# Performance work log

Hardware: AMD Instinct MI355X
Metric: run time of the kernel (lower is better)

The kernel has to match this reference:

```python
import jax, jax.numpy as jnp
import numpy as np

TS = 4  # tile_size


def _disp_upsample_slanted(d, dx, dy, ts):
    """Slanted-plane disparity upsample (PixelShuffle of per-tile-pixel planes).
    d, dx, dy: [B,1,Ht,Wt] -> full-res disparity [B,1,H,W], H=Ht*ts, W=Wt*ts.
    output[y,x] = d[y//ts,x//ts] + (y%ts - c)*dy + (x%ts - c)*dx, c=(ts-1)/2."""
    B, _, Ht, Wt = d.shape
    c = (ts - 1) / 2
    off = jnp.arange(ts, dtype=d.dtype) - jnp.asarray(c, d.dtype)  # [ts]
    d_, dx_, dy_ = d[:, 0], dx[:, 0], dy[:, 0]  # [B,Ht,Wt]
    off_i = off[None, :, None, None, None]  # row offset within tile
    off_j = off[None, None, :, None, None]  # col offset within tile
    disp = d_[:, None, None] + off_i * dy_[:, None, None] + off_j * dx_[:, None, None]
    # [B,ts_i,ts_j,Ht,Wt] -> pixel-shuffle -> [B,1,H,W]
    disp = disp.transpose(0, 3, 1, 4, 2).reshape(B, 1, Ht * ts, Wt * ts)
    return disp


def _l1_cost_chaos(fea_l, fea_r, disp):
    """Per-pixel horizontal warp of fea_r by continuous disparity (linear interp,
    zero outside image), then L1 distance over channels. Returns [B,1,H,W]."""
    B, C, H, W = fea_l.shape
    x = jnp.arange(W, dtype=disp.dtype)
    x_src = x[None, None, None, :] - disp              # [B,1,H,W]
    x0 = jnp.floor(x_src)
    w = (x_src - x0).astype(fea_r.dtype)
    x0i = jnp.clip(x0.astype(jnp.int32), 0, W - 1)
    x1i = jnp.clip(x0i + 1, 0, W - 1)
    f0 = jnp.take_along_axis(fea_r, jnp.broadcast_to(x0i, (B, C, H, W)), axis=3)
    f1 = jnp.take_along_axis(fea_r, jnp.broadcast_to(x1i, (B, C, H, W)), axis=3)
    warped = f0 * (1.0 - w) + f1 * w
    valid = (x_src >= 0) & (x_src <= W - 1)
    warped = jnp.where(valid, warped, jnp.zeros((), fea_r.dtype))
    return jnp.sum(jnp.abs(fea_l - warped), axis=1, keepdims=True)


def _tile_unshuffle(cv, ts):
    """[B,1,H,W] -> [B, ts*ts, H//ts, W//ts]; channel i*ts+j holds cv[i::ts, j::ts]."""
    B, _, H, W = cv.shape
    Ht, Wt = H // ts, W // ts
    return cv.reshape(B, Ht, ts, Wt, ts).transpose(0, 2, 4, 1, 3).reshape(B, ts * ts, Ht, Wt)


def setup_inputs() -> dict:
    key = jax.random.key(0)
    k1, k2, k3, k4, k5 = jax.random.split(key, 5)
    B, C, H, W, ts = 4, 32, 512, 960, TS
    Ht, Wt = H // ts, W // ts
    d = jax.random.uniform(k1, (B, 1, Ht, Wt), jnp.float32) * 48.0
    dx = jax.random.normal(k2, (B, 1, Ht, Wt), jnp.float32) * 0.1
    dy = jax.random.normal(k3, (B, 1, Ht, Wt), jnp.float32) * 0.1
    tile_plane = jnp.concatenate([d, dx, dy], axis=1)  # [B,3,Ht,Wt]
    fea_l = jax.random.normal(k4, (B, C, H, W), jnp.float32)
    fea_r = jax.random.normal(k5, (B, C, H, W), jnp.float32)
    return {"tile_plane": tile_plane, "fea_l": fea_l, "fea_r": fea_r}


def reference(tile_plane, fea_l, fea_r):
    ts = TS
    tile_d = tile_plane[:, 0:1]
    tile_dx = tile_plane[:, 1:2]
    tile_dy = tile_plane[:, 2:3]
    local_cv = []
    for disp_d in (-1, 0, 1):
        disp_full = _disp_upsample_slanted(tile_d + disp_d, tile_dx, tile_dy, ts)
        cv = _l1_cost_chaos(fea_l, fea_r, disp_full)        # [B,1,H,W]
        local_cv.append(_tile_unshuffle(cv, ts))            # [B,ts*ts,Ht,Wt]
    return jnp.concatenate(local_cv, axis=1)                # [B,3*ts*ts,Ht,Wt]
```

## Files before the change

kernel.cpp:

```cpp
#include <hip/hip_runtime.h>
#include <cstdint>

#define AS1 __attribute__((address_space(1)))
#define AS3 __attribute__((address_space(3)))

constexpr int B  = 4;
constexpr int C  = 32;
constexpr int H  = 512;
constexpr int Wd = 960;
constexpr int Ht = H / 4;
constexpr int Wt = Wd / 4;
constexpr int HW = H * Wd;

constexpr int BLKX  = 256;
constexpr int XMARG = 56;
constexpr int SELEM = BLKX + 64;

__global__ __launch_bounds__(256, 4) void tile_warping_kernel(
    const float* __restrict__ tp,
    const float* __restrict__ fl,
    const float* __restrict__ fr,
    float* __restrict__ out)
{
    __shared__ float sm[SELEM * C];

    const int lane = threadIdx.x;
    const int x0 = blockIdx.x * BLKX;
    const int y  = blockIdx.y;
    const int b  = blockIdx.z;
    const int xstart = x0 - XMARG;

    const float* frrow = fr + ((size_t)b * C * H + y) * Wd;
    #pragma unroll
    for (int chunk = 0; chunk < (SELEM * C) / (BLKX * 4); ++chunk) {
        int e   = chunk * (BLKX * 4) + lane * 4;
        int ch  = e / SELEM;
        int off = e - ch * SELEM;
        int gx  = min(max(xstart + off, 0), Wd - 4);
        const float* gp = frrow + (size_t)ch * HW + gx;
        __builtin_amdgcn_global_load_lds((const AS1 float*)gp,
                                         (AS3 float*)(&sm[e]), 16, 0, 0);
    }
    __syncthreads();

    const int x = x0 + lane;
    if (x < Wd) {
        const int ht = y >> 2, ii = y & 3;
        const int wt = x >> 2, jj = x & 3;

        const int tbase = ((b * 3) * Ht + ht) * Wt + wt;
        const float dv  = tp[tbase];
        const float dxv = tp[tbase + Ht * Wt];
        const float dyv = tp[tbase + 2 * Ht * Wt];

        const float oi = (float)ii - 1.5f;
        const float oj = (float)jj - 1.5f;

        int   o0[3];
        float w[3], w1[3];
        bool  val[3];
        #pragma unroll
        for (int k = 0; k < 3; ++k) {
            float disp = ((dv + (float)(k - 1)) + oi * dyv) + oj * dxv;
            float xs = (float)x - disp;
            float ff = floorf(xs);
            w[k]  = xs - ff;
            w1[k] = 1.0f - w[k];
            int c0 = min(max((int)ff, 0), Wd - 1);
            o0[k]  = c0 - xstart;
            val[k] = (xs >= 0.0f) && (xs <= (float)(Wd - 1));
        }

        const float* flp = fl + ((size_t)b * C * H + y) * Wd + x;

        float s0 = 0.f, s1 = 0.f, s2 = 0.f;
        #pragma unroll 4
        for (int c = 0; c < C; ++c) {
            float l = flp[(size_t)c * HW];
            const float* bp = sm + c * SELEM;
            float f00 = bp[o0[0]], f01 = bp[o0[0] + 1];
            float f10 = bp[o0[1]], f11 = bp[o0[1] + 1];
            float f20 = bp[o0[2]], f21 = bp[o0[2] + 1];
            float wv0 = val[0] ? (f00 * w1[0] + f01 * w[0]) : 0.f;
            float wv1 = val[1] ? (f10 * w1[1] + f11 * w[1]) : 0.f;
            float wv2 = val[2] ? (f20 * w1[2] + f21 * w[2]) : 0.f;
            s0 += fabsf(l - wv0);
            s1 += fabsf(l - wv1);
            s2 += fabsf(l - wv2);
        }

        const int obase = ((b * 48) * Ht + ht) * Wt + wt;
        out[obase + (0 * 16 + ii * 4 + jj) * (Ht * Wt)] = s0;
        out[obase + (1 * 16 + ii * 4 + jj) * (Ht * Wt)] = s1;
        out[obase + (2 * 16 + ii * 4 + jj) * (Ht * Wt)] = s2;
    }
}

extern "C" void kernel_launch(void* const* d_in, const int* in_sizes, int n_in,
                              void* d_out, int out_size, void* d_ws, size_t ws_size,
                              hipStream_t stream) {
    const float* tp = (const float*)d_in[0];
    const float* fl = (const float*)d_in[1];
    const float* fr = (const float*)d_in[2];
    float* out = (float*)d_out;

    dim3 grid((Wd + BLKX - 1) / BLKX, H, B);
    tile_warping_kernel<<<grid, 256, 0, stream>>>(tp, fl, fr, out);
}
```

Before: 493.7 us.

## Stage right-feature rows through LDS in two channel phases to raise occupancy

```diff
diff --git a/kernel.cpp b/kernel.cpp
--- a/kernel.cpp
+++ b/kernel.cpp
@@ -15,14 +15,17 @@
 constexpr int BLKX  = 256;
 constexpr int XMARG = 56;
 constexpr int SELEM = BLKX + 64;
+constexpr int CPH   = 16;
+constexpr int NPH   = C / CPH;
+constexpr int NCHUNK = (SELEM * CPH) / (BLKX * 4);
 
-__global__ __launch_bounds__(256, 4) void tile_warping_kernel(
+__global__ __launch_bounds__(256, 7) void tile_warping_kernel(
     const float* __restrict__ tp,
     const float* __restrict__ fl,
     const float* __restrict__ fr,
     float* __restrict__ out)
 {
-    __shared__ float sm[SELEM * C];
+    __shared__ float sm[SELEM * CPH];
 
     const int lane = threadIdx.x;
     const int x0 = blockIdx.x * BLKX;
@@ -31,8 +34,9 @@
     const int xstart = x0 - XMARG;
 
     const float* frrow = fr + ((size_t)b * C * H + y) * Wd;
+
     #pragma unroll
-    for (int chunk = 0; chunk < (SELEM * C) / (BLKX * 4); ++chunk) {
+    for (int chunk = 0; chunk < NCHUNK; ++chunk) {
         int e   = chunk * (BLKX * 4) + lane * 4;
         int ch  = e / SELEM;
         int off = e - ch * SELEM;
@@ -41,13 +45,20 @@
         __builtin_amdgcn_global_load_lds((const AS1 float*)gp,
                                          (AS3 float*)(&sm[e]), 16, 0, 0);
     }
-    __syncthreads();
 
-    const int x = x0 + lane;
-    if (x < Wd) {
-        const int ht = y >> 2, ii = y & 3;
-        const int wt = x >> 2, jj = x & 3;
+    const int x   = x0 + lane;
+    const bool act = (x < Wd);
 
+    const int ht = y >> 2, ii = y & 3;
+    const int wt = x >> 2, jj = x & 3;
+
+    int   o0[3];
+    float w[3], w1[3];
+    bool  val[3];
+    float s0 = 0.f, s1 = 0.f, s2 = 0.f;
+    const float* flp = fl + ((size_t)b * C * H + y) * Wd + x;
+
+    if (act) {
         const int tbase = ((b * 3) * Ht + ht) * Wt + wt;
         const float dv  = tp[tbase];
         const float dxv = tp[tbase + Ht * Wt];
@@ -56,9 +67,6 @@
         const float oi = (float)ii - 1.5f;
         const float oj = (float)jj - 1.5f;
 
-        int   o0[3];
-        float w[3], w1[3];
-        bool  val[3];
         #pragma unroll
         for (int k = 0; k < 3; ++k) {
             float disp = ((dv + (float)(k - 1)) + oi * dyv) + oj * dxv;
@@ -70,25 +78,56 @@
             o0[k]  = c0 - xstart;
             val[k] = (xs >= 0.0f) && (xs <= (float)(Wd - 1));
         }
+    } else {
+        o0[0] = o0[1] = o0[2] = 0;
+        w[0] = w[1] = w[2] = 0.f;
+        w1[0] = w1[1] = w1[2] = 0.f;
+        val[0] = val[1] = val[2] = false;
+    }
 
-        const float* flp = fl + ((size_t)b * C * H + y) * Wd + x;
-
-        float s0 = 0.f, s1 = 0.f, s2 = 0.f;
-        #pragma unroll 4
-        for (int c = 0; c < C; ++c) {
-            float l = flp[(size_t)c * HW];
-            const float* bp = sm + c * SELEM;
-            float f00 = bp[o0[0]], f01 = bp[o0[0] + 1];
-            float f10 = bp[o0[1]], f11 = bp[o0[1] + 1];
-            float f20 = bp[o0[2]], f21 = bp[o0[2] + 1];
-            float wv0 = val[0] ? (f00 * w1[0] + f01 * w[0]) : 0.f;
-            float wv1 = val[1] ? (f10 * w1[1] + f11 * w[1]) : 0.f;
-            float wv2 = val[2] ? (f20 * w1[2] + f21 * w[2]) : 0.f;
-            s0 += fabsf(l - wv0);
-            s1 += fabsf(l - wv1);
-            s2 += fabsf(l - wv2);
+    #pragma unroll
+    for (int p = 0; p < NPH; ++p) {
+        if (p) {
+            __syncthreads();
+            #pragma unroll
+            for (int chunk = 0; chunk < NCHUNK; ++chunk) {
+                int e   = chunk * (BLKX * 4) + lane * 4;
+                int ch  = e / SELEM;
+                int off = e - ch * SELEM;
+                int gx  = min(max(xstart + off, 0), Wd - 4);
+                const float* gp = frrow + (size_t)(p * CPH + ch) * HW + gx;
+                __builtin_amdgcn_global_load_lds((const AS1 float*)gp,
+                                                 (AS3 float*)(&sm[e]), 16, 0, 0);
+            }
         }
 
+        float l[CPH];
+        if (act) {
+            #pragma unroll
+            for (int c = 0; c < CPH; ++c)
+                l[c] = flp[(size_t)(p * CPH + c) * HW];
+        }
+
+        __syncthreads();
+
+        if (act) {
+            #pragma unroll
+            for (int c = 0; c < CPH; ++c) {
+                const float* bp = sm + c * SELEM;
+                float f00 = bp[o0[0]], f01 = bp[o0[0] + 1];
+                float f10 = bp[o0[1]], f11 = bp[o0[1] + 1];
+                float f20 = bp[o0[2]], f21 = bp[o0[2] + 1];
+                float wv0 = val[0] ? (f00 * w1[0] + f01 * w[0]) : 0.f;
+                float wv1 = val[1] ? (f10 * w1[1] + f11 * w[1]) : 0.f;
+                float wv2 = val[2] ? (f20 * w1[2] + f21 * w[2]) : 0.f;
+                s0 += fabsf(l[c] - wv0);
+                s1 += fabsf(l[c] - wv1);
+                s2 += fabsf(l[c] - wv2);
+            }
+        }
+    }
+
+    if (act) {
         const int obase = ((b * 48) * Ht + ht) * Wt + wt;
         out[obase + (0 * 16 + ii * 4 + jj) * (Ht * Wt)] = s0;
         out[obase + (1 * 16 + ii * 4 + jj) * (Ht * Wt)] = s1;
```

After: 850.4 us. 72.3% more time.

## Share one 4-tap LDS window across the three disparities and prefetch fea_l

Applied to the files above, without the earlier changes.

```diff
diff --git a/kernel.cpp b/kernel.cpp
--- a/kernel.cpp
+++ b/kernel.cpp
@@ -15,6 +15,7 @@
 constexpr int BLKX  = 256;
 constexpr int XMARG = 56;
 constexpr int SELEM = BLKX + 64;
+constexpr int NCHUNK = (SELEM * C) / (BLKX * 4);
 
 __global__ __launch_bounds__(256, 4) void tile_warping_kernel(
     const float* __restrict__ tp,
@@ -32,7 +33,7 @@
 
     const float* frrow = fr + ((size_t)b * C * H + y) * Wd;
     #pragma unroll
-    for (int chunk = 0; chunk < (SELEM * C) / (BLKX * 4); ++chunk) {
+    for (int chunk = 0; chunk < NCHUNK; ++chunk) {
         int e   = chunk * (BLKX * 4) + lane * 4;
         int ch  = e / SELEM;
         int off = e - ch * SELEM;
@@ -41,54 +42,74 @@
         __builtin_amdgcn_global_load_lds((const AS1 float*)gp,
                                          (AS3 float*)(&sm[e]), 16, 0, 0);
     }
+
+    const int x   = x0 + lane;
+    const bool act = (x < Wd);
+    const int xc  = act ? x : (Wd - 1);
+
+    const int ht = y >> 2, ii = y & 3;
+    const int wt = xc >> 2, jj = xc & 3;
+
+    const int tbase = ((b * 3) * Ht + ht) * Wt + wt;
+    const float dv  = tp[tbase];
+    const float dxv = tp[tbase + Ht * Wt];
+    const float dyv = tp[tbase + 2 * Ht * Wt];
+
+    const float oi = (float)ii - 1.5f;
+    const float oj = (float)jj - 1.5f;
+
+    const float disp_c = ((dv + 0.0f) + oi * dyv) + oj * dxv;
+    const float xs_c = (float)xc - disp_c;
+    const float xs0 = xs_c + 1.0f;
+    const float xs2 = xs_c - 1.0f;
+
+    const float ff = floorf(xs_c);
+    const float w  = xs_c - ff;
+    const float w1 = 1.0f - w;
+
+    const bool val0 = (xs0  >= 0.0f) && (xs0  <= (float)(Wd - 1));
+    const bool val1 = (xs_c >= 0.0f) && (xs_c <= (float)(Wd - 1));
+    const bool val2 = (xs2  >= 0.0f) && (xs2  <= (float)(Wd - 1));
+
+    const int iw = (int)ff - 1;
+    const int ow = min(max(iw - xstart, 0), SELEM - 4);
+
+    const float* flp = fl + ((size_t)b * C * H + y) * Wd + xc;
+
+    float la[8], lb[8];
+    #pragma unroll
+    for (int j = 0; j < 8; ++j)
+        la[j] = flp[(size_t)j * HW];
+
     __syncthreads();
 
-    const int x = x0 + lane;
-    if (x < Wd) {
-        const int ht = y >> 2, ii = y & 3;
-        const int wt = x >> 2, jj = x & 3;
+    float s0 = 0.f, s1 = 0.f, s2 = 0.f;
 
-        const int tbase = ((b * 3) * Ht + ht) * Wt + wt;
-        const float dv  = tp[tbase];
-        const float dxv = tp[tbase + Ht * Wt];
-        const float dyv = tp[tbase + 2 * Ht * Wt];
-
-        const float oi = (float)ii - 1.5f;
-        const float oj = (float)jj - 1.5f;
-
-        int   o0[3];
-        float w[3], w1[3];
-        bool  val[3];
+    #pragma unroll
+    for (int oct = 0; oct < 4; ++oct) {
+        float* cur = (oct & 1) ? lb : la;
+        float* nxt = (oct & 1) ? la : lb;
+        if (oct < 3) {
+            #pragma unroll
+            for (int j = 0; j < 8; ++j)
+                nxt[j] = flp[(size_t)((oct + 1) * 8 + j) * HW];
+        }
         #pragma unroll
-        for (int k = 0; k < 3; ++k) {
-            float disp = ((dv + (float)(k - 1)) + oi * dyv) + oj * dxv;
-            float xs = (float)x - disp;
-            float ff = floorf(xs);
-            w[k]  = xs - ff;
-            w1[k] = 1.0f - w[k];
-            int c0 = min(max((int)ff, 0), Wd - 1);
-            o0[k]  = c0 - xstart;
-            val[k] = (xs >= 0.0f) && (xs <= (float)(Wd - 1));
-        }
-
-        const float* flp = fl + ((size_t)b * C * H + y) * Wd + x;
-
-        float s0 = 0.f, s1 = 0.f, s2 = 0.f;
-        #pragma unroll 4
-        for (int c = 0; c < C; ++c) {
-            float l = flp[(size_t)c * HW];
-            const float* bp = sm + c * SELEM;
-            float f00 = bp[o0[0]], f01 = bp[o0[0] + 1];
-            float f10 = bp[o0[1]], f11 = bp[o0[1] + 1];
-            float f20 = bp[o0[2]], f21 = bp[o0[2] + 1];
-            float wv0 = val[0] ? (f00 * w1[0] + f01 * w[0]) : 0.f;
-            float wv1 = val[1] ? (f10 * w1[1] + f11 * w[1]) : 0.f;
-            float wv2 = val[2] ? (f20 * w1[2] + f21 * w[2]) : 0.f;
+        for (int j = 0; j < 8; ++j) {
+            const int c = oct * 8 + j;
+            const float* bp = sm + c * SELEM + ow;
+            float t0 = bp[0], t1 = bp[1], t2 = bp[2], t3 = bp[3];
+            float wv0 = val0 ? (t2 * w1 + t3 * w) : 0.f;
+            float wv1 = val1 ? (t1 * w1 + t2 * w) : 0.f;
+            float wv2 = val2 ? (t0 * w1 + t1 * w) : 0.f;
+            float l = cur[j];
             s0 += fabsf(l - wv0);
             s1 += fabsf(l - wv1);
             s2 += fabsf(l - wv2);
         }
+    }
 
+    if (act) {
         const int obase = ((b * 48) * Ht + ht) * Wt + wt;
         out[obase + (0 * 16 + ii * 4 + jj) * (Ht * Wt)] = s0;
         out[obase + (1 * 16 + ii * 4 + jj) * (Ht * Wt)] = s1;
```

Result: slower. 634.8 us (+28.6%).
